# Kernel tuning notes

Measured on AMD Instinct MI355X. Metric: run time of the kernel, lower is better.

## Reference

```python
import jax, jax.numpy as jnp
import numpy as np

N = 50000      # nodes (spots)
E = 800000     # edges (avg degree 16)
G = 1002       # num_genes + 2
D = 256        # latent_dim
C = 20         # num_celltypes
BN_EPS = 1e-5


def setup_inputs() -> dict:
    key = jax.random.key(0)
    ks = jax.random.split(key, 14)
    def p(k, shape, fan_in):
        return (jax.random.normal(k, shape, jnp.float32) / np.sqrt(fan_in)).astype(jnp.float32)
    return {
        "x": jax.random.normal(ks[0], (N, G), jnp.float32),
        "edge_index": jax.random.randint(ks[1], (2, E), 0, N, jnp.int64),
        "lin_w": p(ks[2], (G, D), G),          # encoder Linear (no bias)
        "conv1_w": p(ks[3], (D, D), D),
        "conv1_b": jnp.zeros((D,), jnp.float32),
        "conv2_w": p(ks[4], (D, D), D),
        "conv2_b": jnp.zeros((D,), jnp.float32),
        "mlp1_w": p(ks[5], (D, D), D),
        "mlp1_b": jnp.zeros((D,), jnp.float32),
        "bn_gamma": jnp.ones((D,), jnp.float32),
        "bn_beta": jnp.zeros((D,), jnp.float32),
        "mlp2_w": p(ks[6], (D, C), D),
        "mlp2_b": jnp.zeros((C,), jnp.float32),
    }


def _gcn_conv(x, src, dst, W, b):
    # x: [N, D]; symmetric GCN normalization with self-loops (weight 1)
    n = x.shape[0]
    x = x @ W
    deg = jax.ops.segment_sum(jnp.ones(src.shape[0], x.dtype), dst, num_segments=n) + 1.0
    dinv = jax.lax.rsqrt(deg)
    norm = dinv[src] * dinv[dst]                 # [E]
    agg = jax.ops.segment_sum(norm[:, None] * x[src], dst, num_segments=n)
    agg = agg + x * (1.0 / deg)[:, None]         # self-loop term: deg^-1 * x_i
    return agg + b


def reference(x, edge_index, lin_w, conv1_w, conv1_b, conv2_w, conv2_b,
              mlp1_w, mlp1_b, bn_gamma, bn_beta, mlp2_w, mlp2_b):
    src, dst = edge_index[0], edge_index[1]
    # encoder
    h = x @ lin_w
    h = jax.nn.relu(_gcn_conv(h, src, dst, conv1_w, conv1_b))
    h = jax.nn.relu(_gcn_conv(h, src, dst, conv2_w, conv2_b))
    # decoder MLP (Linear -> BatchNorm(train) -> ReLU -> Linear) + softmax
    h = h @ mlp1_w + mlp1_b
    mu = jnp.mean(h, axis=0)
    var = jnp.var(h, axis=0)
    h = (h - mu) * jax.lax.rsqrt(var + BN_EPS) * bn_gamma + bn_beta
    h = jax.nn.relu(h)
    h = h @ mlp2_w + mlp2_b
    return jax.nn.softmax(h, axis=-1)
```

## Files before the change

### kernel.cpp

```cpp
#include <hip/hip_runtime.h>
#include <cstdint>
#include <cstddef>

typedef unsigned short u16;
typedef unsigned int   u32;
typedef _Float16       f16;
typedef u16  u16x4 __attribute__((ext_vector_type(4)));
typedef u16  u16x8 __attribute__((ext_vector_type(8)));
typedef f16  f16x8 __attribute__((ext_vector_type(8)));
typedef float f32x4 __attribute__((ext_vector_type(4)));

static __device__ __forceinline__ u16 f2h(float f){
  f16 h = (f16)f;
  return __builtin_bit_cast(u16, h);
}
static __device__ __forceinline__ float h2f(u16 b){
  f16 h = __builtin_bit_cast(f16, b);
  return (float)h;
}

static __device__ __forceinline__ void async16(void* lds, const void* g){
  __builtin_amdgcn_global_load_lds(
      (const __attribute__((address_space(1))) u32*)g,
      (__attribute__((address_space(3))) u32*)lds, 16, 0, 0);
}

__global__ void transpose_weights(const float* __restrict__ lw, const float* __restrict__ w1,
                                  const float* __restrict__ w2, const float* __restrict__ w3,
                                  u16* __restrict__ lwT, u16* __restrict__ w1T,
                                  u16* __restrict__ w2T, u16* __restrict__ w3T,
                                  int G, int Gpad)
{
  __shared__ float t[32][33];
  int z = blockIdx.z;
  const float* in = (z==0)? lw : (z==1)? w1 : (z==2)? w2 : w3;
  u16* out        = (z==0)? lwT: (z==1)? w1T: (z==2)? w2T: w3T;
  int R   = (z==0)? G : 256;
  int ldo = (z==0)? Gpad : 256;
  int by = blockIdx.y, bx = blockIdx.x;
  if (by*32 >= R && z != 0) return;
  int tid = threadIdx.x;
  #pragma unroll
  for (int k=0;k<4;k++){
    int p = tid + k*256; int r = p>>5, c = p&31;
    int gr = by*32 + r;
    t[r][c] = (gr < R) ? in[gr*256 + bx*32 + c] : 0.f;
  }
  __syncthreads();
  #pragma unroll
  for (int k=0;k<4;k++){
    int p = tid + k*256; int r = p>>5, c = p&31;
    int oc = by*32 + c;
    if (oc < ldo) out[(bx*32 + r)*ldo + oc] = f2h(t[c][r]);
  }
}

__global__ __launch_bounds__(256) void cast_x(
    const float* __restrict__ x, u16* __restrict__ xh, int N, int G, int Gpad)
{
  int tid = threadIdx.x;
  int r   = blockIdx.x*2 + (tid >> 7);
  int c0  = (tid & 127) * 8;
  if (r >= N) return;
  const float* xr = x + (size_t)r*G;
  u16x8 o;
  if (c0 + 8 <= G){
    #pragma unroll
    for (int k=0;k<4;k++){
      float2 v = *(const float2*)(xr + c0 + k*2);
      o[k*2]   = f2h(v.x);
      o[k*2+1] = f2h(v.y);
    }
  } else {
    #pragma unroll
    for (int j=0;j<8;j++){
      int c = c0 + j;
      o[j] = (c < G) ? f2h(xr[c]) : (u16)0;
    }
  }
  *(u16x8*)(xh + (size_t)r*Gpad + c0) = o;
}

__global__ void count_kernel(const int* __restrict__ dst, int* __restrict__ cnt, int E){
  int e = blockIdx.x*256 + threadIdx.x;
  if (e < E) atomicAdd(&cnt[dst[e]], 1);
}

__global__ void scan_reduce(const int* __restrict__ cnt, int* __restrict__ bsum, int N){
  __shared__ int s[256];
  int tid = threadIdx.x;
  int i = blockIdx.x*256 + tid;
  s[tid] = (i<N)? cnt[i] : 0;
  __syncthreads();
  for (int off=128; off>0; off>>=1){
    if (tid < off) s[tid] += s[tid+off];
    __syncthreads();
  }
  if (tid==0) bsum[blockIdx.x] = s[0];
}

__global__ void scan_offsets(const int* __restrict__ bsum, int* __restrict__ boff, int nb){
  __shared__ int s[256];
  int tid = threadIdx.x;
  int v = (tid<nb)? bsum[tid] : 0;
  s[tid] = v; __syncthreads();
  for (int off=1; off<256; off<<=1){
    int t = (tid>=off)? s[tid-off] : 0;
    __syncthreads();
    s[tid] += t;
    __syncthreads();
  }
  if (tid<nb) boff[tid] = s[tid]-v;
}

__global__ void scan_final(const int* __restrict__ cnt, const int* __restrict__ boff,
                           int* __restrict__ row_ptr, float* __restrict__ dinv, int N, int E){
  __shared__ int s[256];
  int tid = threadIdx.x;
  int i = blockIdx.x*256 + tid;
  int v = (i<N)? cnt[i] : 0;
  s[tid] = v; __syncthreads();
  for (int off=1; off<256; off<<=1){
    int t = (tid>=off)? s[tid-off] : 0;
    __syncthreads();
    s[tid] += t;
    __syncthreads();
  }
  if (i < N){
    row_ptr[i] = boff[blockIdx.x] + s[tid] - v;
    dinv[i] = rsqrtf((float)(v+1));
  }
  if (i == N-1) row_ptr[N] = E;
}

__global__ void scatter_kernel(const int* __restrict__ src, const int* __restrict__ dst,
                               const int* __restrict__ row_ptr, int* __restrict__ cursor,
                               int* __restrict__ colx, int E){
  int e = blockIdx.x*256 + threadIdx.x;
  if (e < E){
    int d = dst[e];
    int pos = atomicAdd(&cursor[d], 1);
    colx[row_ptr[d] + pos] = src[e];
  }
}

template<bool ADD_BIAS>
__global__ __launch_bounds__(256) void gemm_async(
    const u16* __restrict__ Ah,
    const u16* __restrict__ BT, int Kpad,
    u16* __restrict__ C, const float* __restrict__ bias, int M)
{
  __shared__ __align__(16) u16 As[2][4096];
  __shared__ __align__(16) u16 Bs[2][4096];

  const int tid  = threadIdx.x;
  const int lane = tid & 63;
  const int quad = lane >> 4;
  const int l16  = lane & 15;
  const int wave = tid >> 6;
  const int wm = (wave >> 1) << 6;
  const int wn = (wave & 1) << 6;
  const int m0 = blockIdx.y << 7;
  const int n0 = blockIdx.x << 7;

  const u16* bg[2]; u16* lB[2];
  const u16* ag[2]; u16* lA[2];
  #pragma unroll
  for (int i=0;i<2;i++){
    int q = wave*2 + i;
    int rr = lane >> 2, ss = lane & 3;
    int gg = ss ^ ((rr >> 1) & 3);
    bg[i] = BT + (size_t)(n0 + q*16 + rr)*Kpad + gg*8;
    lB[i] = &Bs[0][0] + q*512;
    int gr = m0 + q*16 + rr;
    if (gr >= M) gr = M-1;
    ag[i] = Ah + (size_t)gr*Kpad + gg*8;
    lA[i] = &As[0][0] + q*512;
  }

  auto stage = [&](int buf, int t){
    const int kb = t << 5;
    #pragma unroll
    for (int i=0;i<2;i++) async16(lB[i] + buf*4096, bg[i] + kb);
    #pragma unroll
    for (int i=0;i<2;i++) async16(lA[i] + buf*4096, ag[i] + kb);
  };

  f32x4 acc[4][4];
  #pragma unroll
  for (int i=0;i<4;i++)
    #pragma unroll
    for (int j=0;j<4;j++) acc[i][j] = {0.f,0.f,0.f,0.f};

  const int NT = Kpad >> 5;

  stage(0, 0);
  int cur = 0;
  for (int t=0; t<NT; ++t){
    if (t+1 < NT){
      stage(cur^1, t+1);
      asm volatile("s_waitcnt vmcnt(4)" ::: "memory");
    } else {
      asm volatile("s_waitcnt vmcnt(0)" ::: "memory");
    }
    __builtin_amdgcn_s_barrier();

    const u16* AshC = &As[cur][0];
    const u16* BsC  = &Bs[cur][0];

    f16x8 af[4], bf[4];
    #pragma unroll
    for (int mt=0;mt<4;mt++){
      int R = wm + mt*16 + l16;
      int s = quad ^ ((R >> 1) & 3);
      af[mt] = __builtin_bit_cast(f16x8, *(const u16x8*)(AshC + R*32 + s*8));
    }
    #pragma unroll
    for (int nt=0;nt<4;nt++){
      int R = wn + nt*16 + l16;
      int s = quad ^ ((R >> 1) & 3);
      bf[nt] = __builtin_bit_cast(f16x8, *(const u16x8*)(BsC + R*32 + s*8));
    }
    #pragma unroll
    for (int mt=0;mt<4;mt++)
      #pragma unroll
      for (int nt=0;nt<4;nt++)
        acc[mt][nt] = __builtin_amdgcn_mfma_f32_16x16x32_f16(af[mt], bf[nt], acc[mt][nt], 0, 0, 0);

    __builtin_amdgcn_s_barrier();
    cur ^= 1;
  }

  #pragma unroll
  for (int mt=0;mt<4;mt++){
    #pragma unroll
    for (int nt=0;nt<4;nt++){
      int col = n0 + wn + nt*16 + l16;
      float bv = 0.f;
      if constexpr (ADD_BIAS) bv = bias[col];
      #pragma unroll
      for (int r=0;r<4;r++){
        int row = m0 + wm + mt*16 + quad*4 + r;
        if (row < M) C[(size_t)row*256 + col] = f2h(acc[mt][nt][r] + bv);
      }
    }
  }
}

__global__ __launch_bounds__(256) void agg_kernel(
    const u16* __restrict__ XW, const float* __restrict__ bias,
    const float* __restrict__ dinv, const int* __restrict__ row_ptr,
    const int* __restrict__ colx, u16* __restrict__ H, int N)
{
  int wid = (blockIdx.x << 2) + (threadIdx.x >> 6);
  if (wid >= N) return;
  int lane = threadIdx.x & 63;
  int f = lane << 2;
  float di = dinv[wid];
  int e0 = row_ptr[wid], e1 = row_ptr[wid+1];
  int deg = e1 - e0;
  float a0=0.f, a1=0.f, a2=0.f, a3=0.f;
  for (int base = 0; base < deg; base += 64){
    int mi = 0;
    if (base + lane < deg) mi = colx[e0 + base + lane];
    int cnt = min(deg - base, 64);
    int j = 0;
    for (; j+1 < cnt; j += 2){
      int s0 = __shfl(mi, j);
      int s1 = __shfl(mi, j+1);
      float w0 = dinv[s0]*di;
      float w1 = dinv[s1]*di;
      u16x4 x0 = *(const u16x4*)(XW + (size_t)s0*256 + f);
      u16x4 x1 = *(const u16x4*)(XW + (size_t)s1*256 + f);
      a0 += w0*h2f(x0[0]) + w1*h2f(x1[0]);
      a1 += w0*h2f(x0[1]) + w1*h2f(x1[1]);
      a2 += w0*h2f(x0[2]) + w1*h2f(x1[2]);
      a3 += w0*h2f(x0[3]) + w1*h2f(x1[3]);
    }
    if (j < cnt){
      int s0 = __shfl(mi, j);
      float w0 = dinv[s0]*di;
      u16x4 x0 = *(const u16x4*)(XW + (size_t)s0*256 + f);
      a0 += w0*h2f(x0[0]); a1 += w0*h2f(x0[1]);
      a2 += w0*h2f(x0[2]); a3 += w0*h2f(x0[3]);
    }
  }
  u16x4 xs = *(const u16x4*)(XW + (size_t)wid*256 + f);
  float wd = di*di;
  a0 += wd*h2f(xs[0]); a1 += wd*h2f(xs[1]); a2 += wd*h2f(xs[2]); a3 += wd*h2f(xs[3]);
  const float4 bb = *(const float4*)(bias + f);
  a0 = fmaxf(a0 + bb.x, 0.f);
  a1 = fmaxf(a1 + bb.y, 0.f);
  a2 = fmaxf(a2 + bb.z, 0.f);
  a3 = fmaxf(a3 + bb.w, 0.f);
  u16x4 o = { f2h(a0), f2h(a1), f2h(a2), f2h(a3) };
  *(u16x4*)(H + (size_t)wid*256 + f) = o;
}

__global__ void bn_stats(const u16* __restrict__ H, float* __restrict__ bsum,
                         float* __restrict__ bsq, int N){
  int col = threadIdx.x;
  float s=0.f, q=0.f;
  for (int r=blockIdx.x; r<N; r+=gridDim.x){
    float v = h2f(H[(size_t)r*256 + col]);
    s += v; q += v*v;
  }
  atomicAdd(&bsum[col], s);
  atomicAdd(&bsq[col], q);
}

__global__ void bn_finalize(const float* __restrict__ bsum, const float* __restrict__ bsq,
                            const float* __restrict__ gamma, const float* __restrict__ beta,
                            float* __restrict__ scale, float* __restrict__ shift, int N){
  int c = threadIdx.x;
  float invN = 1.f/(float)N;
  float mu  = bsum[c]*invN;
  float var = bsq[c]*invN - mu*mu;
  float sc  = gamma[c] * rsqrtf(var + 1e-5f);
  scale[c] = sc;
  shift[c] = beta[c] - mu*sc;
}

__global__ __launch_bounds__(256) void final_kernel(
    const u16* __restrict__ H, const float* __restrict__ scale, const float* __restrict__ shift,
    const float* __restrict__ W2, const float* __restrict__ b2, float* __restrict__ out, int N)
{
  __shared__ float W2s[256*20];
  __shared__ float scs[256];
  __shared__ float shs[256];
  __shared__ float b2s[20];
  int tid = threadIdx.x;
  for (int i=tid; i<5120; i+=256) W2s[i] = W2[i];
  scs[tid] = scale[tid];
  shs[tid] = shift[tid];
  if (tid < 20) b2s[tid] = b2[tid];
  __syncthreads();
  int r = blockIdx.x*256 + tid;
  if (r >= N) return;
  float l[20];
  #pragma unroll
  for (int c=0;c<20;c++) l[c] = b2s[c];
  const u16* hrow = H + (size_t)r*256;
  for (int j0=0;j0<256;j0+=8){
    u16x8 h8 = *(const u16x8*)(hrow + j0);
    #pragma unroll
    for (int t=0;t<8;t++){
      int j = j0+t;
      float a = fmaxf(fmaf(h2f(h8[t]), scs[j], shs[j]), 0.f);
      const float* wr = W2s + j*20;
      #pragma unroll
      for (int c=0;c<20;c++) l[c] = fmaf(a, wr[c], l[c]);
    }
  }
  float m = l[0];
  #pragma unroll
  for (int c=1;c<20;c++) m = fmaxf(m, l[c]);
  float ssum = 0.f;
  #pragma unroll
  for (int c=0;c<20;c++){ l[c] = __expf(l[c]-m); ssum += l[c]; }
  float inv = 1.f/ssum;
  float* orow = out + (size_t)r*20;
  #pragma unroll
  for (int c=0;c<20;c++) orow[c] = l[c]*inv;
}

extern "C" void kernel_launch(void* const* d_in, const int* in_sizes, int n_in,
                              void* d_out, int out_size, void* d_ws, size_t ws_size,
                              hipStream_t stream)
{
  (void)n_in; (void)out_size; (void)ws_size;
  const float* x     = (const float*)d_in[0];
  const int*   ei    = (const int*)d_in[1];
  const float* lin_w = (const float*)d_in[2];
  const float* c1w   = (const float*)d_in[3];
  const float* c1b   = (const float*)d_in[4];
  const float* c2w   = (const float*)d_in[5];
  const float* c2b   = (const float*)d_in[6];
  const float* m1w   = (const float*)d_in[7];
  const float* m1b   = (const float*)d_in[8];
  const float* gam   = (const float*)d_in[9];
  const float* bet   = (const float*)d_in[10];
  const float* m2w   = (const float*)d_in[11];
  const float* m2b   = (const float*)d_in[12];
  float* out = (float*)d_out;

  const int E = in_sizes[1]/2;
  const int G = in_sizes[2]/256;
  const int N = in_sizes[0]/G;
  const int Gpad = (G + 31) & ~31;
  const int* srcI = ei;
  const int* dstI = ei + E;

  char* w = (char*)d_ws;
  auto alloc = [&](size_t bytes)->char*{
    char* p = w;
    w += (bytes + 255) & ~(size_t)255;
    return p;
  };
  u16* Ha    = (u16*)alloc((size_t)N*256*2);
  u16* Hb    = (u16*)alloc((size_t)N*256*2);
  u16* xh    = (u16*)alloc((size_t)N*Gpad*2);
  u16* linT  = (u16*)alloc((size_t)256*Gpad*2);
  u16* w1T   = (u16*)alloc(256*256*2);
  u16* w2T   = (u16*)alloc(256*256*2);
  u16* w3T   = (u16*)alloc(256*256*2);
  int* cnt    = (int*)alloc((size_t)N*4);
  int* cursor = (int*)alloc((size_t)N*4);
  int* rowp   = (int*)alloc((size_t)(N+1)*4);
  int* colx   = (int*)alloc((size_t)E*4);
  float* dinv = (float*)alloc((size_t)N*4);
  int* bsum   = (int*)alloc(1024);
  int* boff   = (int*)alloc(1024);
  float* bnsum= (float*)alloc(1024);
  float* bnsq = (float*)alloc(1024);
  float* scl  = (float*)alloc(1024);
  float* shf  = (float*)alloc(1024);

  hipMemsetAsync(cnt,    0, (size_t)N*4, stream);
  hipMemsetAsync(cursor, 0, (size_t)N*4, stream);
  hipMemsetAsync(bnsum,  0, 2048, stream);

  const int NB = (N + 255)/256;

  transpose_weights<<<dim3(8, Gpad>>5, 4), 256, 0, stream>>>(
      lin_w, c1w, c2w, m1w, linT, w1T, w2T, w3T, G, Gpad);
  cast_x<<<dim3((N+1)/2), 256, 0, stream>>>(x, xh, N, G, Gpad);
  count_kernel  <<<dim3((E+255)/256), 256, 0, stream>>>(dstI, cnt, E);
  scan_reduce   <<<dim3(NB), 256, 0, stream>>>(cnt, bsum, N);
  scan_offsets  <<<dim3(1),  256, 0, stream>>>(bsum, boff, NB);
  scan_final    <<<dim3(NB), 256, 0, stream>>>(cnt, boff, rowp, dinv, N, E);
  scatter_kernel<<<dim3((E+255)/256), 256, 0, stream>>>(srcI, dstI, rowp, cursor, colx, E);

  dim3 ggrid(2, (N+127)/128);
  gemm_async<false><<<ggrid, 256, 0, stream>>>(xh, linT, Gpad, Ha, nullptr, N);
  gemm_async<false><<<ggrid, 256, 0, stream>>>(Ha, w1T,  256,  Hb, nullptr, N);
  agg_kernel<<<dim3((N+3)/4), 256, 0, stream>>>(Hb, c1b, dinv, rowp, colx, Ha, N);
  gemm_async<false><<<ggrid, 256, 0, stream>>>(Ha, w2T,  256,  Hb, nullptr, N);
  agg_kernel<<<dim3((N+3)/4), 256, 0, stream>>>(Hb, c2b, dinv, rowp, colx, Ha, N);
  gemm_async<true ><<<ggrid, 256, 0, stream>>>(Ha, w3T,  256,  Hb, m1b, N);
  bn_stats   <<<dim3(256), 256, 0, stream>>>(Hb, bnsum, bnsq, N);
  bn_finalize<<<dim3(1),   256, 0, stream>>>(bnsum, bnsq, gam, bet, scl, shf, N);
  final_kernel<<<dim3(NB), 256, 0, stream>>>(Hb, scl, shf, m2w, m2b, out, N);
}
```

Before: 725.6 us.

## Fold encoder weight into conv1 weight and unroll aggregation gather by four

Precomputes lin_w @ conv1_w as a single Gpad x 256 fp16 weight, using a small GEMM that writes its result transposed. The two back-to-back large GEMMs over all N nodes become one, removing a full N x 256 intermediate write and read plus a 256-deep GEMM pass. The aggregation loop now processes four neighbors per iteration to keep more gathers in flight. The product is rounded to fp16 before the big GEMM, which slightly changes numerics.

```diff
diff --git a/kernel.cpp b/kernel.cpp
--- a/kernel.cpp
+++ b/kernel.cpp
@@ -25,57 +25,57 @@
       (__attribute__((address_space(3))) u32*)lds, 16, 0, 0);
 }
 
-__global__ void transpose_weights(const float* __restrict__ lw, const float* __restrict__ w1,
-                                  const float* __restrict__ w2, const float* __restrict__ w3,
-                                  u16* __restrict__ lwT, u16* __restrict__ w1T,
-                                  u16* __restrict__ w2T, u16* __restrict__ w3T,
-                                  int G, int Gpad)
+__global__ void transpose_weights(const float* __restrict__ w1, const float* __restrict__ w2,
+                                  const float* __restrict__ w3,
+                                  u16* __restrict__ w1T, u16* __restrict__ w2T,
+                                  u16* __restrict__ w3T)
 {
   __shared__ float t[32][33];
   int z = blockIdx.z;
-  const float* in = (z==0)? lw : (z==1)? w1 : (z==2)? w2 : w3;
-  u16* out        = (z==0)? lwT: (z==1)? w1T: (z==2)? w2T: w3T;
-  int R   = (z==0)? G : 256;
-  int ldo = (z==0)? Gpad : 256;
+  const float* in = (z==0)? w1 : (z==1)? w2 : w3;
+  u16* out        = (z==0)? w1T: (z==1)? w2T: w3T;
   int by = blockIdx.y, bx = blockIdx.x;
-  if (by*32 >= R && z != 0) return;
   int tid = threadIdx.x;
   #pragma unroll
   for (int k=0;k<4;k++){
     int p = tid + k*256; int r = p>>5, c = p&31;
-    int gr = by*32 + r;
-    t[r][c] = (gr < R) ? in[gr*256 + bx*32 + c] : 0.f;
+    t[r][c] = in[(by*32 + r)*256 + bx*32 + c];
   }
   __syncthreads();
   #pragma unroll
   for (int k=0;k<4;k++){
     int p = tid + k*256; int r = p>>5, c = p&31;
-    int oc = by*32 + c;
-    if (oc < ldo) out[(bx*32 + r)*ldo + oc] = f2h(t[c][r]);
-  }
-}
-
-__global__ __launch_bounds__(256) void cast_x(
-    const float* __restrict__ x, u16* __restrict__ xh, int N, int G, int Gpad)
-{
-  int tid = threadIdx.x;
-  int r   = blockIdx.x*2 + (tid >> 7);
-  int c0  = (tid & 127) * 8;
-  if (r >= N) return;
-  const float* xr = x + (size_t)r*G;
+    out[(bx*32 + r)*256 + by*32 + c] = f2h(t[c][r]);
+  }
+}
+
+__global__ __launch_bounds__(256) void cast_pad(
+    const float* __restrict__ x, u16* __restrict__ xh, int N, int Npad, int G, int Gpad)
+{
+  int tid = threadIdx.x;
+  int tpr = Gpad >> 3;
+  int r   = blockIdx.x*(256/tpr) + tid/tpr;
+  if (r >= Npad) return;
+  int c0  = (tid % tpr) * 8;
   u16x8 o;
-  if (c0 + 8 <= G){
-    #pragma unroll
-    for (int k=0;k<4;k++){
-      float2 v = *(const float2*)(xr + c0 + k*2);
-      o[k*2]   = f2h(v.x);
-      o[k*2+1] = f2h(v.y);
-    }
+  if (r >= N){
+    #pragma unroll
+    for (int j=0;j<8;j++) o[j] = 0;
   } else {
-    #pragma unroll
-    for (int j=0;j<8;j++){
-      int c = c0 + j;
-      o[j] = (c < G) ? f2h(xr[c]) : (u16)0;
+    const float* xr = x + (size_t)r*G;
+    if (c0 + 8 <= G){
+      #pragma unroll
+      for (int k=0;k<4;k++){
+        float2 v = *(const float2*)(xr + c0 + k*2);
+        o[k*2]   = f2h(v.x);
+        o[k*2+1] = f2h(v.y);
+      }
+    } else {
+      #pragma unroll
+      for (int j=0;j<8;j++){
+        int c = c0 + j;
+        o[j] = (c < G) ? f2h(xr[c]) : (u16)0;
+      }
     }
   }
   *(u16x8*)(xh + (size_t)r*Gpad + c0) = o;
@@ -144,11 +144,11 @@
   }
 }
 
-template<bool ADD_BIAS>
+template<bool ADD_BIAS, bool STORE_T>
 __global__ __launch_bounds__(256) void gemm_async(
     const u16* __restrict__ Ah,
     const u16* __restrict__ BT, int Kpad,
-    u16* __restrict__ C, const float* __restrict__ bias, int M)
+    u16* __restrict__ C, const float* __restrict__ bias, int M, int ldc)
 {
   __shared__ __align__(16) u16 As[2][4096];
   __shared__ __align__(16) u16 Bs[2][4096];
@@ -231,17 +231,32 @@
     cur ^= 1;
   }
 
-  #pragma unroll
-  for (int mt=0;mt<4;mt++){
-    #pragma unroll
-    for (int nt=0;nt<4;nt++){
-      int col = n0 + wn + nt*16 + l16;
-      float bv = 0.f;
-      if constexpr (ADD_BIAS) bv = bias[col];
-      #pragma unroll
-      for (int r=0;r<4;r++){
-        int row = m0 + wm + mt*16 + quad*4 + r;
-        if (row < M) C[(size_t)row*256 + col] = f2h(acc[mt][nt][r] + bv);
+  if constexpr (STORE_T){
+    #pragma unroll
+    for (int mt=0;mt<4;mt++){
+      #pragma unroll
+      for (int nt=0;nt<4;nt++){
+        int col  = n0 + wn + nt*16 + l16;
+        int row0 = m0 + wm + mt*16 + quad*4;
+        u16x4 o;
+        #pragma unroll
+        for (int r=0;r<4;r++) o[r] = f2h(acc[mt][nt][r]);
+        if (row0 < M) *(u16x4*)(C + (size_t)col*ldc + row0) = o;
+      }
+    }
+  } else {
+    #pragma unroll
+    for (int mt=0;mt<4;mt++){
+      #pragma unroll
+      for (int nt=0;nt<4;nt++){
+        int col = n0 + wn + nt*16 + l16;
+        float bv = 0.f;
+        if constexpr (ADD_BIAS) bv = bias[col];
+        #pragma unroll
+        for (int r=0;r<4;r++){
+          int row = m0 + wm + mt*16 + quad*4 + r;
+          if (row < M) C[(size_t)row*256 + col] = f2h(acc[mt][nt][r] + bv);
+        }
       }
     }
   }
@@ -265,19 +280,25 @@
     if (base + lane < deg) mi = colx[e0 + base + lane];
     int cnt = min(deg - base, 64);
     int j = 0;
-    for (; j+1 < cnt; j += 2){
+    for (; j+3 < cnt; j += 4){
       int s0 = __shfl(mi, j);
       int s1 = __shfl(mi, j+1);
+      int s2 = __shfl(mi, j+2);
+      int s3 = __shfl(mi, j+3);
       float w0 = dinv[s0]*di;
       float w1 = dinv[s1]*di;
+      float w2 = dinv[s2]*di;
+      float w3 = dinv[s3]*di;
       u16x4 x0 = *(const u16x4*)(XW + (size_t)s0*256 + f);
       u16x4 x1 = *(const u16x4*)(XW + (size_t)s1*256 + f);
-      a0 += w0*h2f(x0[0]) + w1*h2f(x1[0]);
-      a1 += w0*h2f(x0[1]) + w1*h2f(x1[1]);
-      a2 += w0*h2f(x0[2]) + w1*h2f(x1[2]);
-      a3 += w0*h2f(x0[3]) + w1*h2f(x1[3]);
-    }
-    if (j < cnt){
+      u16x4 x2 = *(const u16x4*)(XW + (size_t)s2*256 + f);
+      u16x4 x3 = *(const u16x4*)(XW + (size_t)s3*256 + f);
+      a0 += w0*h2f(x0[0]) + w1*h2f(x1[0]) + w2*h2f(x2[0]) + w3*h2f(x3[0]);
+      a1 += w0*h2f(x0[1]) + w1*h2f(x1[1]) + w2*h2f(x2[1]) + w3*h2f(x3[1]);
+      a2 += w0*h2f(x0[2]) + w1*h2f(x1[2]) + w2*h2f(x2[2]) + w3*h2f(x3[2]);
+      a3 += w0*h2f(x0[3]) + w1*h2f(x1[3]) + w2*h2f(x2[3]) + w3*h2f(x3[3]);
+    }
+    for (; j < cnt; ++j){
       int s0 = __shfl(mi, j);
       float w0 = dinv[s0]*di;
       u16x4 x0 = *(const u16x4*)(XW + (size_t)s0*256 + f);
@@ -400,7 +421,8 @@
   u16* Ha    = (u16*)alloc((size_t)N*256*2);
   u16* Hb    = (u16*)alloc((size_t)N*256*2);
   u16* xh    = (u16*)alloc((size_t)N*Gpad*2);
-  u16* linT  = (u16*)alloc((size_t)256*Gpad*2);
+  u16* linH  = (u16*)alloc((size_t)Gpad*256*2);
+  u16* BT1   = (u16*)alloc((size_t)256*Gpad*2);
   u16* w1T   = (u16*)alloc(256*256*2);
   u16* w2T   = (u16*)alloc(256*256*2);
   u16* w3T   = (u16*)alloc(256*256*2);
@@ -422,9 +444,12 @@
 
   const int NB = (N + 255)/256;
 
-  transpose_weights<<<dim3(8, Gpad>>5, 4), 256, 0, stream>>>(
-      lin_w, c1w, c2w, m1w, linT, w1T, w2T, w3T, G, Gpad);
-  cast_x<<<dim3((N+1)/2), 256, 0, stream>>>(x, xh, N, G, Gpad);
+  transpose_weights<<<dim3(8, 8, 3), 256, 0, stream>>>(c1w, c2w, m1w, w1T, w2T, w3T);
+  cast_pad<<<dim3((Gpad+7)/8), 256, 0, stream>>>(lin_w, linH, G, Gpad, 256, 256);
+  cast_pad<<<dim3((N+1)/2), 256, 0, stream>>>(x, xh, N, N, G, Gpad);
+  gemm_async<false, true><<<dim3(2, Gpad/128), 256, 0, stream>>>(
+      linH, w1T, 256, BT1, nullptr, Gpad, Gpad);
+
   count_kernel  <<<dim3((E+255)/256), 256, 0, stream>>>(dstI, cnt, E);
   scan_reduce   <<<dim3(NB), 256, 0, stream>>>(cnt, bsum, N);
   scan_offsets  <<<dim3(1),  256, 0, stream>>>(bsum, boff, NB);
@@ -432,12 +457,11 @@
   scatter_kernel<<<dim3((E+255)/256), 256, 0, stream>>>(srcI, dstI, rowp, cursor, colx, E);
 
   dim3 ggrid(2, (N+127)/128);
-  gemm_async<false><<<ggrid, 256, 0, stream>>>(xh, linT, Gpad, Ha, nullptr, N);
-  gemm_async<false><<<ggrid, 256, 0, stream>>>(Ha, w1T,  256,  Hb, nullptr, N);
+  gemm_async<false, false><<<ggrid, 256, 0, stream>>>(xh, BT1, Gpad, Hb, nullptr, N, 256);
   agg_kernel<<<dim3((N+3)/4), 256, 0, stream>>>(Hb, c1b, dinv, rowp, colx, Ha, N);
-  gemm_async<false><<<ggrid, 256, 0, stream>>>(Ha, w2T,  256,  Hb, nullptr, N);
+  gemm_async<false, false><<<ggrid, 256, 0, stream>>>(Ha, w2T, 256, Hb, nullptr, N, 256);
   agg_kernel<<<dim3((N+3)/4), 256, 0, stream>>>(Hb, c2b, dinv, rowp, colx, Ha, N);
-  gemm_async<true ><<<ggrid, 256, 0, stream>>>(Ha, w3T,  256,  Hb, m1b, N);
+  gemm_async<true, false><<<ggrid, 256, 0, stream>>>(Ha, w3T, 256, Hb, m1b, N, 256);
   bn_stats   <<<dim3(256), 256, 0, stream>>>(Hb, bnsum, bnsq, N);
   bn_finalize<<<dim3(1),   256, 0, stream>>>(bnsum, bnsq, gam, bet, scl, shf, N);
   final_kernel<<<dim3(NB), 256, 0, stream>>>(Hb, scl, shf, m2w, m2b, out, N);
```

New measurement: 706.9 us. 2.6% less time.
